# Kernel optimization log

Hardware: AMD Instinct MI355X
Metric: run time of the kernel (lower is better)

Reference implementation:

```python
import jax, jax.numpy as jnp
import numpy as np

N = 6144       # nodes
E = 98304      # edges (~16 per node)
D = 256        # input_dim
K = 20         # max_clusters
NUM_LVS = 32   # distinct LV group ids
MIN_SIZE = 3.0
MAX_SIZE = 20.0


def _lv_constraint_table():
    # Static per-LV preferred-cluster soft constraint (0.3 base, 1.0 preferred).
    max_cpl = max(2, K // max(1, NUM_LVS - 5))
    table = np.ones((NUM_LVS, K), dtype=np.float32)
    for i in range(NUM_LVS):
        start = (i * 2) % K
        end = min(start + max_cpl, K)
        pref = np.zeros(K, dtype=np.float32)
        pref[start:end] = 1.0
        table[i] = 0.3 + 0.7 * pref
    return jnp.asarray(table)

_LV_TABLE = _lv_constraint_table()


def _apply_size_constraints(S):
    cs = S.sum(axis=0)  # soft cluster sizes [K]
    pen = jnp.zeros_like(cs)
    pen = jnp.where(cs > MAX_SIZE, -jnp.log(cs / MAX_SIZE + 1e-8), pen)
    pen = jnp.where((cs > 0) & (cs < MIN_SIZE), -0.5 * jnp.log(cs / MIN_SIZE + 1e-8), pen)
    S_adj = jax.nn.softmax(jnp.log(S + 1e-8) + pen[None, :], axis=1)
    very_over = cs > MAX_SIZE * 1.5
    for k in range(K):  # K is small & static; sequential like the original
        col = S_adj[:, k]
        thr = jnp.quantile(col, 0.7)
        weak = (col < thr) & very_over[k]
        S_adj = S_adj.at[:, k].set(jnp.where(weak, 0.0, col))
        rs = jnp.sum(jnp.abs(S_adj), axis=1, keepdims=True)
        S_adj = jnp.where(weak[:, None], S_adj / jnp.maximum(rs, 1e-12), S_adj)
    return jnp.where(jnp.any(pen != 0.0), S_adj, S)


def _hard_rebalance(S):
    n = S.shape[0]
    for _ in range(5):  # fixed max_iterations (early-break is a no-op via masks)
        cs = S.sum(axis=0)  # stale within the k-loop, as in the original
        very_over = cs > MAX_SIZE
        for k in range(K):
            excess = cs[k] - MAX_SIZE
            active = very_over[k] & (excess > 0)
            col = S[:, k]
            num = jnp.minimum(jnp.ceil(excess).astype(jnp.int32) + 5, n)
            order = jnp.argsort(col)  # ascending: weakest first
            ranks = jnp.zeros((n,), jnp.int32).at[order].set(jnp.arange(n, dtype=jnp.int32))
            weak = (ranks < num) & active
            S = S.at[:, k].set(jnp.where(weak, 1e-8, col))
            avail = jnp.clip(MAX_SIZE - cs, 0.0, None)
            w = avail / (avail.sum() + 1e-8)
            S = jnp.where(weak[:, None], S + w[None, :] * S[:, k:k + 1], S)
            rs = jnp.sum(jnp.abs(S), axis=1, keepdims=True)
            S = jnp.where(weak[:, None], S / jnp.maximum(rs, 1e-12), S)
    return S


def _forward(x, edge_index, lv_group_ids, W1, b1, W2, b2, W3, b3, We1, be1, We2, be2):
    n = x.shape[0]
    # assign_net (dropout is identity in eval)
    h = jax.nn.relu(x @ W1 + b1)
    h = jax.nn.relu(h @ W2 + b2)
    logits = h @ W3 + b3  # [N, K]

    # LV mask: values in {0.3, 1.0}; masked_fill only triggers on exact zeros (kept faithful)
    lv_sizes = jax.ops.segment_sum(jnp.ones((n,), logits.dtype), lv_group_ids, num_segments=NUM_LVS)
    big = (lv_sizes > 30.0)[lv_group_ids]
    lv_mask = jnp.where(big[:, None], _LV_TABLE[lv_group_ids], 1.0)
    logits = jnp.where(lv_mask == 0.0, -1e9, logits)

    # load-balancing regularization (reconstructed; source truncated)
    S_soft = jax.nn.softmax(logits, axis=1)
    target = n / K
    logits = logits - 0.1 * (S_soft.sum(axis=0) - target)[None, :] / target

    S = jax.nn.softmax(logits, axis=1)
    S = _apply_size_constraints(S)
    S = _hard_rebalance(S)

    x_embed = jax.nn.relu(x @ We1 + be1) @ We2 + be2
    x_pooled = S.T @ x_embed  # [K, D]

    adj = jnp.zeros((n, n), x.dtype).at[edge_index[0], edge_index[1]].set(1.0)
    adj_pooled = S.T @ adj @ S  # [K, K]

    # link prediction loss: BCE(S S^T, adj) with torch's log clamp at -100
    p = jnp.clip(S @ S.T, 0.0, 1.0)
    logp = jnp.maximum(jnp.log(p), -100.0)
    log1mp = jnp.maximum(jnp.log1p(-p), -100.0)
    link_loss = -jnp.mean(adj * logp + (1.0 - adj) * log1mp)

    entropy_loss = -jnp.mean(jnp.sum(S * jnp.log(S + 1e-8), axis=1))
    balance_loss = jnp.mean(jnp.abs(S.sum(axis=0) - target)) / target
    aux = link_loss + 0.1 * entropy_loss + 0.5 * balance_loss
    return x_pooled, adj_pooled, S, aux


def setup_inputs() -> dict:
    key = jax.random.key(0)
    ks = jax.random.split(key, 8)
    x = jax.random.normal(ks[0], (N, D), jnp.float32)
    edge_index = jax.random.randint(ks[1], (2, E), 0, N)
    lv_group_ids = jax.random.randint(ks[2], (N,), 0, NUM_LVS)

    def lin(k, fi, fo):
        k1, k2 = jax.random.split(k)
        lim = 1.0 / np.sqrt(fi)
        return (jax.random.uniform(k1, (fi, fo), jnp.float32, -lim, lim),
                jax.random.uniform(k2, (fo,), jnp.float32, -lim, lim))

    W1, b1 = lin(ks[3], D, D // 2)
    W2, b2 = lin(ks[4], D // 2, D // 4)
    W3 = jax.random.normal(ks[5], (D // 4, K), jnp.float32) * 0.1  # _init_balanced_assignment
    b3 = jnp.zeros((K,), jnp.float32)
    We1, be1 = lin(ks[6], D, D)
    We2, be2 = lin(ks[7], D, D)
    return dict(x=x, edge_index=edge_index, lv_group_ids=lv_group_ids,
                W1=W1, b1=b1, W2=W2, b2=b2, W3=W3, b3=b3,
                We1=We1, be1=be1, We2=We2, be2=be2)


def reference(x, edge_index, lv_group_ids, W1, b1, W2, b2, W3, b3, We1, be1, We2, be2):
    return _forward(x, edge_index, lv_group_ids, W1, b1, W2, b2, W3, b3, We1, be1, We2, be2)
```

## Files before the change

kernel.cpp:

```cpp
#include <hip/hip_runtime.h>
#include <math.h>

#define N_NODES 6144
#define KCL 20
#define NE 98304
#define RPT 6

#define OFF_BITMAP   491520ull
#define OFF_COLSUM0  5210112ull
#define OFF_CSG      5210192ull
#define OFF_CSFIN    5210272ull
#define OFF_DACC     5210368ull
#define OFF_TICK     5210400ull
#define HDR_BYTES    296ull
#define OFF_LOGITS   5210624ull
#define OFF_WEAK     5235200ull
#define OFF_CSS      5358080ull
#define OFF_TOTZ     5358160ull
#define OFF_UCM      5702144ull
#define OFF_XE       6685184ull
#define OFF_GOUT     13001216ull
#define OFF_RWS      13025792ull

__global__ __launch_bounds__(128) void k_mlp(const float* __restrict__ x,
    const float* __restrict__ W1, const float* __restrict__ b1,
    const float* __restrict__ W2, const float* __restrict__ b2,
    const float* __restrict__ W3, const float* __restrict__ b3,
    float* __restrict__ logits, float* __restrict__ colsum0,
    unsigned* __restrict__ bitmap, float* __restrict__ outHead){
  __shared__ float xs[16][256];
  __shared__ float h1[16][128];
  __shared__ float h2[16][64];
  __shared__ float logitsL[16][20];
  __shared__ float csL[20];
  const int tid = threadIdx.x;
  const int r0 = blockIdx.x * 16;
  { uint4* bm4 = (uint4*)bitmap;
    const int base = blockIdx.x*128 + tid;
    const uint4 z = make_uint4(0u,0u,0u,0u);
    #pragma unroll
    for (int i=0;i<6;i++) bm4[base + i*49152] = z; }
  if (blockIdx.x==0){ for (int i=tid;i<5520;i+=128) outHead[i]=0.f; }
  if (tid < 20) csL[tid]=0.f;
  for (int idx = tid; idx < 16*256; idx += 128){ int u = idx >> 8, i = idx & 255; xs[u][i] = x[(r0+u)*256 + i]; }
  __syncthreads();
  {
    float acc[16]; float bb = b1[tid];
    #pragma unroll
    for (int u=0;u<16;u++) acc[u]=bb;
    for (int i=0;i<256;i++){ float wv = W1[i*128+tid];
      #pragma unroll
      for (int u=0;u<16;u++) acc[u]=fmaf(xs[u][i], wv, acc[u]); }
    #pragma unroll
    for (int u=0;u<16;u++) h1[u][tid]=fmaxf(acc[u],0.f);
  }
  __syncthreads();
  if (tid < 64){
    float acc[16]; float bb = b2[tid];
    #pragma unroll
    for (int u=0;u<16;u++) acc[u]=bb;
    for (int i=0;i<128;i++){ float wv = W2[i*64+tid];
      #pragma unroll
      for (int u=0;u<16;u++) acc[u]=fmaf(h1[u][i], wv, acc[u]); }
    #pragma unroll
    for (int u=0;u<16;u++) h2[u][tid]=fmaxf(acc[u],0.f);
  }
  __syncthreads();
  if (tid < 20){
    float acc[16]; float bb = b3[tid];
    #pragma unroll
    for (int u=0;u<16;u++) acc[u]=bb;
    for (int i=0;i<64;i++){ float wv = W3[i*20+tid];
      #pragma unroll
      for (int u=0;u<16;u++) acc[u]=fmaf(h2[u][i], wv, acc[u]); }
    #pragma unroll
    for (int u=0;u<16;u++){ logits[(r0+u)*20+tid]=acc[u]; logitsL[u][tid]=acc[u]; }
  }
  __syncthreads();
  if (tid < 16){
    float y[20]; float m=-INFINITY;
    #pragma unroll
    for (int c=0;c<20;c++){ y[c]=logitsL[tid][c]; m=fmaxf(m,y[c]); }
    float s=0.f;
    #pragma unroll
    for (int c=0;c<20;c++){ y[c]=expf(y[c]-m); s+=y[c]; }
    #pragma unroll
    for (int c=0;c<20;c++) atomicAdd(&csL[c], y[c]/s);
  }
  __syncthreads();
  if (tid < 20) atomicAdd(&colsum0[tid], csL[tid]);
}

__global__ __launch_bounds__(256) void k_sm2cm(const float* __restrict__ logits, const float* __restrict__ colsum0,
    float* __restrict__ Ucm, float* __restrict__ csG){
  __shared__ float adjv[20]; __shared__ float csL[20];
  const int tid = threadIdx.x;
  if (tid < 20){ adjv[tid] = (0.1f*(colsum0[tid]-307.2f))/307.2f; csL[tid]=0.f; }
  __syncthreads();
  const int r = blockIdx.x*256 + tid;
  float y[20]; float m=-INFINITY;
  const float4* lp = (const float4*)(logits + r*20);
  #pragma unroll
  for (int q=0;q<5;q++){ float4 f=lp[q]; y[q*4]=f.x; y[q*4+1]=f.y; y[q*4+2]=f.z; y[q*4+3]=f.w; }
  #pragma unroll
  for (int c=0;c<20;c++){ y[c]=y[c]-adjv[c]; m=fmaxf(m,y[c]); }
  float s=0.f;
  #pragma unroll
  for (int c=0;c<20;c++){ y[c]=expf(y[c]-m); s+=y[c]; }
  #pragma unroll
  for (int c=0;c<20;c++){ float v=y[c]/s; Ucm[c*6144+r]=v; atomicAdd(&csL[c], v); }
  __syncthreads();
  if (tid < 20) atomicAdd(&csG[tid], csL[tid]);
}

__global__ __launch_bounds__(256) void k_prep(const float* __restrict__ csG,
    float* __restrict__ Ucm, float* __restrict__ Rws){
  const int r = blockIdx.x*256 + threadIdx.x;
  float pen[20]; int flag=0;
  #pragma unroll
  for (int c=0;c<20;c++){ float cc=csG[c]; float p=0.f;
    if (cc > 20.0f) p = -logf(cc/20.0f + 1e-8f);
    if (cc > 0.0f && cc < 3.0f) p = -0.5f*logf(cc/3.0f + 1e-8f);
    pen[c]=p; if (p != 0.f) flag=1; }
  float y[20];
  #pragma unroll
  for (int c=0;c<20;c++) y[c]=Ucm[c*6144+r];
  float ts=0.f;
  if (flag){
    float m2=-INFINITY;
    #pragma unroll
    for (int c=0;c<20;c++){ y[c]=logf(y[c]+1e-8f)+pen[c]; m2=fmaxf(m2,y[c]); }
    float s2=0.f;
    #pragma unroll
    for (int c=0;c<20;c++){ y[c]=expf(y[c]-m2); s2+=y[c]; }
    #pragma unroll
    for (int c=0;c<20;c++){ float vv=y[c]/s2; Ucm[c*6144+r]=vv; ts+=vv; }
  } else {
    #pragma unroll
    for (int c=0;c<20;c++) ts+=y[c];
  }
  Rws[r]=ts;
}


__device__ __forceinline__ void load6(const float* p, float* v){
  const float2* q = (const float2*)p;
  float2 a=q[0], b=q[1], c=q[2];
  v[0]=a.x; v[1]=a.y; v[2]=b.x; v[3]=b.y; v[4]=c.x; v[5]=c.y;
}

struct MidShared {
  unsigned hist[2048*8];
  unsigned pad[3000];
  double wred[16*20];
  int wT20[16][20]; int wB20[16][20]; int totZ20[20];
  float csGs[20]; float csS[20];
  unsigned st[8];
  alignas(16) unsigned wMin[16];
  alignas(16) int wS[16];
};

__device__ __forceinline__ int blockExclScan16(int val, int tid, int lane, int wv,
                                               int* wS, int* totOut){
  __syncthreads();
  int inc = val;
  for (int off=1;off<64;off<<=1){ int nv=__shfl_up(inc,off); if (lane>=off) inc+=nv; }
  if (lane==63) wS[wv]=inc;
  __syncthreads();
  int4 a=*(int4*)&wS[0], b=*(int4*)&wS[4], c=*(int4*)&wS[8], d=*(int4*)&wS[12];
  int tot = a.x+a.y+a.z+a.w + b.x+b.y+b.z+b.w + c.x+c.y+c.z+c.w + d.x+d.y+d.z+d.w;
  int base = 0;
  base += (wv> 0)?a.x:0; base += (wv> 1)?a.y:0; base += (wv> 2)?a.z:0; base += (wv> 3)?a.w:0;
  base += (wv> 4)?b.x:0; base += (wv> 5)?b.y:0; base += (wv> 6)?b.z:0; base += (wv> 7)?b.w:0;
  base += (wv> 8)?c.x:0; base += (wv> 9)?c.y:0; base += (wv>10)?c.z:0; base += (wv>11)?c.w:0;
  base += (wv>12)?d.x:0; base += (wv>13)?d.y:0; base += (wv>14)?d.z:0;
  *totOut = tot;
  return base + inc - val;
}

struct SelRes { unsigned kv, below, rankin, ties; };

__device__ SelRes selectKth6(const float* v, int rank0, unsigned* hist,
                             unsigned* st, int* wS, int tid, int lane, int wv){
  unsigned st0=0u, st1=0u, st2=(unsigned)rank0, st3=0u;
  const unsigned rep=(unsigned)(lane&7);
  bool done=false;
  for (int p=0;p<3 && !done;p++){
    const int shift=(p==0)?21:((p==1)?10:0);
    const int bins =(p==2)?1024:2048;
    unsigned bb[RPT];
    #pragma unroll
    for (int u=0;u<RPT;u++){
      unsigned key=__float_as_uint(v[u]);
      bool ok=(p==0);
      if (p==1) ok=((key>>21)==(st0>>21));
      if (p==2) ok=((key>>10)==(st0>>10));
      bb[u]= ok ? ((key>>shift)&(unsigned)(bins-1)) : 0xFFFFFFFFu;
    }
    #pragma unroll
    for (int u=0;u<RPT;u++){
      bool first=(bb[u]!=0xFFFFFFFFu);
      #pragma unroll
      for (int j=0;j<u;j++) first = first && (bb[j]!=bb[u]);
      if (first){
        unsigned cnt=1u;
        #pragma unroll
        for (int j=u+1;j<RPT;j++) cnt += (bb[j]==bb[u]) ? 1u:0u;
        atomicAdd(&hist[(bb[u]<<3)+rep], cnt);
      }
// ... 137 lines not shown
  { float2* gp = (float2*)(G2 + r0);
    gp[0]=make_float2(G[0],G[1]); gp[1]=make_float2(G[2],G[3]); gp[2]=make_float2(G[4],G[5]); }
  { float2* rp = (float2*)(Rws + r0);
    rp[0]=make_float2(R[0],R[1]); rp[1]=make_float2(R[2],R[3]); rp[2]=make_float2(R[4],R[5]); }
}

__device__ void embed_block(MidShared& sm, const float* __restrict__ x,
    const float* __restrict__ We1, const float* __restrict__ be1,
    const float* __restrict__ We2, const float* __restrict__ be2,
    float* __restrict__ xe, int blk){
  float (*xs)[256] = (float (*)[256])(sm.hist);
  float (*h)[256]  = (float (*)[256])(sm.hist + 4096);
  const int tid = threadIdx.x;
  const int col = tid & 255;
  const int ug  = tid >> 8;
  const int r0 = blk * 16;
  { float4* xsf4 = (float4*)xs;
    xsf4[tid] = ((const float4*)(x + r0*256))[tid]; }
  __syncthreads();
  float acc[4];
  { float bb = be1[col];
    #pragma unroll
    for (int u=0;u<4;u++) acc[u]=bb; }
  for (int i=0;i<256;i+=4){
    float w0 = We1[(i+0)*256+col];
    float w1 = We1[(i+1)*256+col];
    float w2 = We1[(i+2)*256+col];
    float w3 = We1[(i+3)*256+col];
    #pragma unroll
    for (int u=0;u<4;u++){
      const float4 xv = *(const float4*)&xs[ug*4+u][i];
      acc[u]=fmaf(xv.x, w0, acc[u]);
      acc[u]=fmaf(xv.y, w1, acc[u]);
      acc[u]=fmaf(xv.z, w2, acc[u]);
      acc[u]=fmaf(xv.w, w3, acc[u]);
    }
  }
  #pragma unroll
  for (int u=0;u<4;u++) h[ug*4+u][col]=fmaxf(acc[u],0.f);
  __syncthreads();
  { float bb = be2[col];
    #pragma unroll
    for (int u=0;u<4;u++) acc[u]=bb; }
  for (int i=0;i<256;i+=4){
    float w0 = We2[(i+0)*256+col];
    float w1 = We2[(i+1)*256+col];
    float w2 = We2[(i+2)*256+col];
    float w3 = We2[(i+3)*256+col];
    #pragma unroll
    for (int u=0;u<4;u++){
      const float4 xv = *(const float4*)&h[ug*4+u][i];
      acc[u]=fmaf(xv.x, w0, acc[u]);
      acc[u]=fmaf(xv.y, w1, acc[u]);
      acc[u]=fmaf(xv.z, w2, acc[u]);
      acc[u]=fmaf(xv.w, w3, acc[u]);
    }
  }
  #pragma unroll
  for (int u=0;u<4;u++) xe[(r0+ug*4+u)*256+col]=acc[u];
}

__global__ __launch_bounds__(1024) void k_midwide(const float* __restrict__ csG,
    float* __restrict__ Rws, float* __restrict__ G2,
    float* __restrict__ Ucm,
    const float* __restrict__ x,
    const float* __restrict__ We1, const float* __restrict__ be1,
    const float* __restrict__ We2, const float* __restrict__ be2,
    float* __restrict__ xe,
    const int* __restrict__ ei, unsigned int* __restrict__ bitmap){
  __shared__ MidShared sm;
  const int blk = blockIdx.x;
  if (blk == 0){
    constr_block(sm, csG, Rws, G2, Ucm);
  } else if (blk <= 384){
    embed_block(sm, x, We1, be1, We2, be2, xe, blk-1);
  } else {
    const int e = (blk-385)*1024 + threadIdx.x;
    const int i = ei[e], j = ei[NE+e];
    unsigned bit = (unsigned)i*6144u + (unsigned)j;
    atomicOr(&bitmap[bit >> 5], 1u << (bit & 31u));
  }
}

__global__ __launch_bounds__(1024) void k_rbA(const float* __restrict__ G2,
    const float* __restrict__ Ucm, float* __restrict__ csS, int* __restrict__ totZ,
    unsigned char* __restrict__ weak){
  __shared__ double wredL[16];
  __shared__ int wTL[16];
  const int c = blockIdx.x;
  const int tid = threadIdx.x;
  const int lane = tid & 63, wv = tid >> 6;
  const int r0 = tid*RPT;
  float vv[RPT], g[RPT];
  load6(Ucm + c*6144 + r0, vv);
  load6(G2 + r0, g);
  double d=0.0; int z=0;
  #pragma unroll
  for (int u=0;u<RPT;u++){
    if (vv[u]==0.0f) z++;
    d += (double)__fmul_rn(vv[u], g[u]);
  }
  for (int off=32;off>0;off>>=1) d += __shfl_down(d, off);
  int inc=z;
  for (int off=1;off<64;off<<=1){ int nv=__shfl_up(inc,off); if (lane>=off) inc+=nv; }
  if (lane==0)  wredL[wv]=d;
  if (lane==63) wTL[wv]=inc;
  __syncthreads();
  double s=0.0;
  #pragma unroll
  for (int w2=0;w2<16;w2++) s += wredL[w2];
  const float cs=(float)s;
  int base=0, tz=0;
  #pragma unroll
  for (int w2=0;w2<16;w2++){ int t=wTL[w2]; if (w2<wv) base+=t; tz+=t; }
  int num=(int)ceilf(cs-20.0f)+5; if (num>6144) num=6144;
  const bool act = (cs > 20.0f);
  int rank = base + inc - z;
  #pragma unroll
  for (int u=0;u<RPT;u++){
    bool zb = (vv[u]==0.0f);
    weak[c*6144 + r0 + u] = (act && zb && rank<num) ? (unsigned char)1 : (unsigned char)0;
    if (zb) rank++;
  }
  if (tid==0){ csS[c]=cs; totZ[c]=tz; }
}

__global__ __launch_bounds__(1024) void k_rbC(float* __restrict__ G2,
    float* __restrict__ Rws, float* __restrict__ Ucm,
    const float* __restrict__ csS, const int* __restrict__ totZ,
    const unsigned char* __restrict__ weak){
  __shared__ MidShared sm;
  const int tid = threadIdx.x;
  float csL[20]; float s0=0.f; unsigned actm=0u;
  #pragma unroll
  for (int c=0;c<20;c++){ float cs=csS[c]; csL[c]=cs;
    s0 += fmaxf(20.0f-cs,0.f);
    if (cs > 20.0f) actm |= (1u<<c); }
  const int wzero=(s0==0.0f)?1:0;
  const float wsum=s0+1e-8f;
  const int anyA=(actm!=0u)?1:0;
  int ng=0;
  #pragma unroll
  for (int c=0;c<20;c++){
    if ((actm>>c)&1u){
      int num=(int)ceilf(csL[c]-20.0f)+5; if (num>6144) num=6144;
      if (num > totZ[c]) ng=1;
    }
  }
  if (anyA && !wzero) ng=1;
  if (!anyA) return;
  if (!ng){
    const int r = blockIdx.x*1024 + tid;
    float G=G2[r], R=Rws[r];
    #pragma unroll
    for (int c=0;c<20;c++){
      if (weak[c*6144+r]){
        float Gold = G;
        float t   = __fadd_rn(__fmul_rn(R, Gold), 1e-8f);
        float rsm = fmaxf(t, 1e-12f);
        float un  = __fdiv_rn(1e-8f, Gold);
        Ucm[c*6144+r] = un;
        G = __fdiv_rn(Gold, rsm);
        R = __fadd_rn(R, un);
      }
    }
    G2[r]=G; Rws[r]=R;
  } else {
    if (blockIdx.x!=0) return;
    unsigned* hist = sm.hist; unsigned* st = sm.st; int* wS = sm.wS;
    const int lane = tid & 63, wv = tid >> 6;
    const int r0 = tid*RPT;
    { uint4* h4=(uint4*)hist; const uint4 z=make_uint4(0u,0u,0u,0u);
      #pragma unroll
      for (int i=0;i<4;i++) h4[tid+i*1024]=z; }
    __syncthreads();
    float G[RPT], R[RPT];
    load6(G2 + r0, G);
    load6(Rws + r0, R);
    for (int k=0;k<20;k++){
      if ((actm>>k)&1u){
        float cs=csL[k];
        int num=(int)ceilf(cs-20.0f)+5; if (num>6144) num=6144;
        float u24[RPT];
        load6(Ucm + k*6144 + r0, u24);
        int zc=0;
        #pragma unroll
        for (int u=0;u<RPT;u++) zc += (u24[u]==0.0f) ? 1 : 0;
        int tz2;
        int zBase = blockExclScan16(zc, tid, lane, wv, wS, &tz2);
        bool wk[RPT];
        if (num <= tz2){
          int cnt = zBase;
          #pragma unroll
          for (int u=0;u<RPT;u++){ wk[u]=false; if (u24[u]==0.0f){ if (cnt<num) wk[u]=true; cnt++; } }
        } else {
          float sv24[RPT];
          #pragma unroll
          for (int u=0;u<RPT;u++) sv24[u]=__fmul_rn(u24[u], G[u]);
          SelRes sr = selectKth6(sv24, num-1, hist, st, wS, tid, lane, wv);
          unsigned kV = sr.kv;
          int L = (int)sr.below;
          int Rq = num - L;
          int ec=0;
          #pragma unroll
          for (int u=0;u<RPT;u++) ec += (__float_as_uint(sv24[u])==kV) ? 1 : 0;
          int eTot;
          int eBase = blockExclScan16(ec, tid, lane, wv, wS, &eTot);
          int cnt = eBase;
          #pragma unroll
          for (int u=0;u<RPT;u++){
            unsigned key = __float_as_uint(sv24[u]); wk[u]=false;
            if (key < kV) wk[u]=true;
            else if (key == kV){ if (cnt < Rq) wk[u]=true; cnt++; }
          }
        }
        #pragma unroll
        for (int u=0;u<RPT;u++){
          if (wk[u]){
            const int r = r0+u;
            float rs=0.f; float xv2[20];
            #pragma unroll
            for (int j=0;j<20;j++){
              float xv = (j==k) ? 1e-8f : __fmul_rn(Ucm[j*6144+r], G[u]);
              float wLj = fmaxf(20.0f - csL[j], 0.f) / wsum;
              xv = __fadd_rn(xv, __fmul_rn(wLj, 1e-8f));
              xv2[j]=xv; rs += fabsf(xv);
            }
            float rsm = fmaxf(rs, 1e-12f);
            float nR = 0.f;
            #pragma unroll
            for (int j=0;j<20;j++){
              float nv = __fdiv_rn(xv2[j], rsm);
              Ucm[j*6144+r] = nv; nR += nv;
            }
            G[u]=1.0f; R[u]=nR;
          }
        }
        __syncthreads();
      }
    }
    { float2* gp = (float2*)(G2 + r0);
      gp[0]=make_float2(G[0],G[1]); gp[1]=make_float2(G[2],G[3]); gp[2]=make_float2(G[4],G[5]); }
    { float2* rp = (float2*)(Rws + r0);
      rp[0]=make_float2(R[0],R[1]); rp[1]=make_float2(R[2],R[3]); rp[2]=make_float2(R[4],R[5]); }
  }
}

__global__ __launch_bounds__(256) void k_tail1(const float* __restrict__ Ucm,
    const float* __restrict__ Gout, const float* __restrict__ xe,
    const unsigned* __restrict__ bitmap,
    float* __restrict__ outXP, float* __restrict__ outS,
    float* __restrict__ csfin, double* __restrict__ dAcc,
    float* __restrict__ outAdj, float* __restrict__ outAux,
    unsigned* __restrict__ ticket){
  __shared__ float SiT[256][21];
  __shared__ float SjT[256][21];
  __shared__ float csL[20];
  __shared__ float adjacc[400];
  __shared__ double wsum[4];
  const int tid = threadIdx.x;
  const int blk = blockIdx.x;
  const int lane = tid & 63, wvq = tid >> 6;

  if (blk < 24){
    const int r0 = blk * 256;
    if (tid < 20) csL[tid]=0.f;
    __syncthreads();
    {
      const int r = r0 + tid;
      const float Gr = Gout[r];
      float sv[20]; float ent=0.f;
      #pragma unroll
      for (int c=0;c<20;c++) sv[c]=__fmul_rn(Ucm[c*6144+r], Gr);
      float4* so = (float4*)(outS + r*20);
      #pragma unroll
      for (int q=0;q<5;q++){ float4 f; f.x=sv[q*4]; f.y=sv[q*4+1]; f.z=sv[q*4+2]; f.w=sv[q*4+3]; so[q]=f; }
      #pragma unroll
      for (int c=0;c<20;c++){ SiT[tid][c]=sv[c]; ent += sv[c]*logf(sv[c]+1e-08f); }
      #pragma unroll
      for (int c=0;c<20;c++) atomicAdd(&csL[c], sv[c]);
      double ed = (double)ent;
      for (int off=32;off>0;off>>=1) ed += __shfl_down(ed, off);
      if (lane==0) wsum[wvq]=ed;
    }
    __syncthreads();
    if (tid==0) atomicAdd(&dAcc[2], wsum[0]+wsum[1]+wsum[2]+wsum[3]);
    if (tid<20) atomicAdd(&csfin[tid], csL[tid]);
    float acc[20];
    #pragma unroll
    for (int c=0;c<20;c++) acc[c]=0.f;
    for (int i=0;i<256;i++){
      float xv = xe[(r0+i)*256 + tid];
      #pragma unroll
      for (int c=0;c<20;c++) acc[c]=fmaf(SiT[i][c], xv, acc[c]);
    }
    #pragma unroll
    for (int c=0;c<20;c++) atomicAdd(&outXP[c*256+tid], acc[c]);
  } else if (blk < 120){
    const int rbase = (blk-24)*64 + wvq*16;
    for (int t=tid;t<400;t+=256) adjacc[t]=0.f;
    __syncthreads();
    int c7[7], d7[7], n7=0;
    #pragma unroll
    for (int q=0;q<7;q++){ int e=lane+64*q; if (e<400){ c7[q]=e/20; d7[q]=e%20; n7=q+1; } }
    float acc7[7];
    #pragma unroll
    for (int q=0;q<7;q++) acc7[q]=0.f;
    float eacc = 0.f;
    for (int rr=0; rr<16; rr++){
      const int i = rbase + rr;
      const float Gi = Gout[i];
      float Si[20];
      #pragma unroll
      for (int c=0;c<20;c++) Si[c]=__fmul_rn(Ucm[c*6144+i], Gi);
      float Tp[20];
      #pragma unroll
      for (int c=0;c<20;c++) Tp[c]=0.f;
      #pragma unroll
      for (int w=0; w<3; w++){
        const int wq = lane + w*64;
        unsigned word = bitmap[i*192 + wq];
        while (word){
          int b = __ffs((int)word) - 1; word &= (word-1u);
          int j = wq*32 + b;
          const float Gj = Gout[j];
          float p = 0.f;
          #pragma unroll
          for (int c=0;c<20;c++){
// ... 22 lines not shown
    #pragma unroll
    for (int q=0;q<7;q++){
      if (q < n7) atomicAdd(&adjacc[lane+64*q], acc7[q]);
    }
    double cd = (double)eacc;
    for (int off=32;off>0;off>>=1) cd += __shfl_down(cd, off);
    if (lane==0) wsum[wvq]=cd;
    __syncthreads();
    if (tid==0) atomicAdd(&dAcc[1], wsum[0]+wsum[1]+wsum[2]+wsum[3]);
    for (int t=tid;t<400;t+=256) atomicAdd(&outAdj[t], adjacc[t]);
  } else {
    const int q2 = blk - 120;
    const int ib = (q2/24)*256, jb = (q2%24)*256;
    const float gi = Gout[ib+tid];
    #pragma unroll
    for (int c=0;c<20;c++) SiT[tid][c] = __fmul_rn(Ucm[c*6144+ib+tid], gi);
    const float gj = Gout[jb+tid];
    #pragma unroll
    for (int c=0;c<20;c++) SjT[tid][c] = __fmul_rn(Ucm[c*6144+jb+tid], gj);
    __syncthreads();
    float rA[20];
    #pragma unroll
    for (int c=0;c<20;c++) rA[c]=SiT[tid][c];
    float af = 0.f;
    for (int jj=0;jj<256;jj++){
      float p=0.f;
      #pragma unroll
      for (int c=0;c<20;c++) p = fmaf(rA[c], SjT[jj][c], p);
      float pcl = fminf(fmaxf(p,0.f),1.f);
      af += fmaxf(__logf(1.0f-pcl), -100.f);
    }
    double cd = (double)af;
    for (int off=32;off>0;off>>=1) cd += __shfl_down(cd, off);
    if (lane==0) wsum[wvq]=cd;
    __syncthreads();
    if (tid==0) atomicAdd(&dAcc[0], wsum[0]+wsum[1]+wsum[2]+wsum[3]);
  }

  __syncthreads();
  if (tid==0){
    unsigned t = atomicAdd(ticket, 1u);
    if (t == 695u){
      __threadfence();
      double l0 = __hip_atomic_load(&dAcc[0], __ATOMIC_RELAXED, __HIP_MEMORY_SCOPE_AGENT);
      double l1 = __hip_atomic_load(&dAcc[1], __ATOMIC_RELAXED, __HIP_MEMORY_SCOPE_AGENT);
      double l2 = __hip_atomic_load(&dAcc[2], __ATOMIC_RELAXED, __HIP_MEMORY_SCOPE_AGENT);
      float s=0.f;
      for (int c=0;c<20;c++){
        float cf = __hip_atomic_load(&csfin[c], __ATOMIC_RELAXED, __HIP_MEMORY_SCOPE_AGENT);
        s += fabsf(cf-307.2f);
      }
      const double nsq = 6144.0*6144.0;
      float link = (float)(-(l0+l1)/nsq);
      float ent  = (float)(-(l2/6144.0));
      float bal = (s/20.0f)/307.2f;
      outAux[0] = link + 0.1f*ent + 0.5f*bal;
    }
  }
}

extern "C" void kernel_launch(void* const* d_in, const int* in_sizes, int n_in,
                              void* d_out, int out_size, void* d_ws, size_t ws_size,
                              hipStream_t stream) {
  const float* x   = (const float*)d_in[0];
  const int*   ei  = (const int*)d_in[1];
  const float* W1  = (const float*)d_in[3];
  const float* b1  = (const float*)d_in[4];
  const float* W2  = (const float*)d_in[5];
  const float* b2  = (const float*)d_in[6];
  const float* W3  = (const float*)d_in[7];
  const float* b3  = (const float*)d_in[8];
  const float* We1 = (const float*)d_in[9];
  const float* be1 = (const float*)d_in[10];
  const float* We2 = (const float*)d_in[11];
  const float* be2 = (const float*)d_in[12];

  char* ws = (char*)d_ws;
  unsigned int* bitmap = (unsigned int*)(ws + OFF_BITMAP);
  float* colsum0  = (float*)(ws + OFF_COLSUM0);
  float* csG      = (float*)(ws + OFF_CSG);
  float* csfin    = (float*)(ws + OFF_CSFIN);
  double* dAcc    = (double*)(ws + OFF_DACC);
  unsigned* ticket= (unsigned*)(ws + OFF_TICK);
  float* logits   = (float*)(ws + OFF_LOGITS);
  float* Ucm      = (float*)(ws + OFF_UCM);
  float* xe       = (float*)(ws + OFF_XE);
  float* Rws      = (float*)(ws + OFF_RWS);
  float* G2       = logits;
  unsigned char* weak = (unsigned char*)(ws + OFF_WEAK);
  float* csS      = (float*)(ws + OFF_CSS);
  int*   totZ     = (int*)(ws + OFF_TOTZ);

  float* out   = (float*)d_out;
  float* outXP = out;
  float* outAdj= out + 5120;
  float* outS  = out + 5520;
  float* outAux= out + 128400;

  hipMemsetAsync(ws + OFF_COLSUM0, 0, (size_t)HDR_BYTES, stream);

  k_mlp<<<384, 128, 0, stream>>>(x, W1,b1, W2,b2, W3,b3, logits, colsum0, bitmap, out);
  k_sm2cm<<<24, 256, 0, stream>>>(logits, colsum0, Ucm, csG);
  k_prep<<<24, 256, 0, stream>>>(csG, Ucm, Rws);
  k_midwide<<<481, 1024, 0, stream>>>(csG, Rws, G2, Ucm,
                                      x, We1, be1, We2, be2, xe, ei, bitmap);
  for (int it=0; it<5; ++it){
    k_rbA<<<20, 1024, 0, stream>>>(G2, Ucm, csS, totZ, weak);
    k_rbC<<<6, 1024, 0, stream>>>(G2, Rws, Ucm, csS, totZ, weak);
  }
  k_tail1<<<696, 256, 0, stream>>>(Ucm, G2, xe, bitmap,
                                   outXP, outS, csfin, dAcc, outAdj, outAux, ticket);
}
```

Before: 528.1 us.

## Fuse rebalance loop and softmax/prep kernels using software grid barriers

Replaces the ten small per-iteration rebalance launches with one persistent 20-block kernel that runs all five iterations, using an atomic-counter grid barrier between phases. The softmax and size-penalty prep kernels are likewise merged with a grid barrier, and the softmax values are kept in registers instead of being reloaded from Ucm. The goal is to remove launch overhead and inter-kernel gaps on a latency-bound chain. In exchange it relies on all blocks being co-resident, and spin-waiting adds some cost; the barrier counters are zeroed by the extended header memset.

```diff
diff --git a/kernel.cpp b/kernel.cpp
--- a/kernel.cpp
+++ b/kernel.cpp
@@ -12,14 +12,15 @@
 #define OFF_CSFIN    5210272ull
 #define OFF_DACC     5210368ull
 #define OFF_TICK     5210400ull
-#define HDR_BYTES    296ull
+#define OFF_GBAR     5210404ull
+#define OFF_GBAR2    5210408ull
+#define HDR_BYTES    304ull
 #define OFF_LOGITS   5210624ull
 #define OFF_WEAK     5235200ull
 #define OFF_CSS      5358080ull
 #define OFF_TOTZ     5358160ull
 #define OFF_UCM      5702144ull
 #define OFF_XE       6685184ull
-#define OFF_GOUT     13001216ull
 #define OFF_RWS      13025792ull
 
 __global__ __launch_bounds__(128) void k_mlp(const float* __restrict__ x,
@@ -91,8 +92,9 @@
   if (tid < 20) atomicAdd(&colsum0[tid], csL[tid]);
 }
 
-__global__ __launch_bounds__(256) void k_sm2cm(const float* __restrict__ logits, const float* __restrict__ colsum0,
-    float* __restrict__ Ucm, float* __restrict__ csG){
+__global__ __launch_bounds__(256) void k_sm2p(const float* __restrict__ logits,
+    const float* __restrict__ colsum0, float* __restrict__ Ucm,
+    float* __restrict__ csG, float* __restrict__ Rws, unsigned* __restrict__ gbar2){
   __shared__ float adjv[20]; __shared__ float csL[20];
   const int tid = threadIdx.x;
   if (tid < 20){ adjv[tid] = (0.1f*(colsum0[tid]-307.2f))/307.2f; csL[tid]=0.f; }
@@ -108,23 +110,24 @@
   #pragma unroll
   for (int c=0;c<20;c++){ y[c]=expf(y[c]-m); s+=y[c]; }
   #pragma unroll
-  for (int c=0;c<20;c++){ float v=y[c]/s; Ucm[c*6144+r]=v; atomicAdd(&csL[c], v); }
+  for (int c=0;c<20;c++){ float v=y[c]/s; y[c]=v; Ucm[c*6144+r]=v; atomicAdd(&csL[c], v); }
   __syncthreads();
   if (tid < 20) atomicAdd(&csG[tid], csL[tid]);
-}
-
-__global__ __launch_bounds__(256) void k_prep(const float* __restrict__ csG,
-    float* __restrict__ Ucm, float* __restrict__ Rws){
-  const int r = blockIdx.x*256 + threadIdx.x;
+  __syncthreads();
+  if (tid==0){
+    __threadfence();
+    __hip_atomic_fetch_add(gbar2, 1u, __ATOMIC_RELEASE, __HIP_MEMORY_SCOPE_AGENT);
+    while (__hip_atomic_load(gbar2, __ATOMIC_ACQUIRE, __HIP_MEMORY_SCOPE_AGENT) < 24u)
+      __builtin_amdgcn_s_sleep(2);
+    __threadfence();
+  }
+  __syncthreads();
   float pen[20]; int flag=0;
   #pragma unroll
   for (int c=0;c<20;c++){ float cc=csG[c]; float p=0.f;
     if (cc > 20.0f) p = -logf(cc/20.0f + 1e-8f);
     if (cc > 0.0f && cc < 3.0f) p = -0.5f*logf(cc/3.0f + 1e-8f);
     pen[c]=p; if (p != 0.f) flag=1; }
-  float y[20];
-  #pragma unroll
-  for (int c=0;c<20;c++) y[c]=Ucm[c*6144+r];
   float ts=0.f;
   if (flag){
     float m2=-INFINITY;
@@ -428,167 +431,185 @@
   }
 }
 
-__global__ __launch_bounds__(1024) void k_rbA(const float* __restrict__ G2,
-    const float* __restrict__ Ucm, float* __restrict__ csS, int* __restrict__ totZ,
-    unsigned char* __restrict__ weak){
+__device__ __forceinline__ void gridbar20(unsigned* gbar, unsigned target){
+  __syncthreads();
+  if (threadIdx.x==0){
+    __threadfence();
+    __hip_atomic_fetch_add(gbar, 1u, __ATOMIC_RELEASE, __HIP_MEMORY_SCOPE_AGENT);
+    while (__hip_atomic_load(gbar, __ATOMIC_ACQUIRE, __HIP_MEMORY_SCOPE_AGENT) < target)
+      __builtin_amdgcn_s_sleep(4);
+    __threadfence();
+  }
+  __syncthreads();
+}
+
+__global__ __launch_bounds__(1024) void k_rebal5(float* __restrict__ G2,
+    float* __restrict__ Rws, float* __restrict__ Ucm,
+    float* __restrict__ csS, int* __restrict__ totZ,
+    unsigned char* __restrict__ weak, unsigned* __restrict__ gbar){
+  __shared__ MidShared sm;
   __shared__ double wredL[16];
   __shared__ int wTL[16];
-  const int c = blockIdx.x;
   const int tid = threadIdx.x;
   const int lane = tid & 63, wv = tid >> 6;
-  const int r0 = tid*RPT;
-  float vv[RPT], g[RPT];
-  load6(Ucm + c*6144 + r0, vv);
-  load6(G2 + r0, g);
-  double d=0.0; int z=0;
-  #pragma unroll
-  for (int u=0;u<RPT;u++){
-    if (vv[u]==0.0f) z++;
-    d += (double)__fmul_rn(vv[u], g[u]);
-  }
-  for (int off=32;off>0;off>>=1) d += __shfl_down(d, off);
-  int inc=z;
-  for (int off=1;off<64;off<<=1){ int nv=__shfl_up(inc,off); if (lane>=off) inc+=nv; }
-  if (lane==0)  wredL[wv]=d;
-  if (lane==63) wTL[wv]=inc;
-  __syncthreads();
-  double s=0.0;
-  #pragma unroll
-  for (int w2=0;w2<16;w2++) s += wredL[w2];
-  const float cs=(float)s;
-  int base=0, tz=0;
-  #pragma unroll
-  for (int w2=0;w2<16;w2++){ int t=wTL[w2]; if (w2<wv) base+=t; tz+=t; }
-  int num=(int)ceilf(cs-20.0f)+5; if (num>6144) num=6144;
-  const bool act = (cs > 20.0f);
-  int rank = base + inc - z;
-  #pragma unroll
-  for (int u=0;u<RPT;u++){
-    bool zb = (vv[u]==0.0f);
-    weak[c*6144 + r0 + u] = (act && zb && rank<num) ? (unsigned char)1 : (unsigned char)0;
-    if (zb) rank++;
-  }
-  if (tid==0){ csS[c]=cs; totZ[c]=tz; }
-}
-
-__global__ __launch_bounds__(1024) void k_rbC(float* __restrict__ G2,
-    float* __restrict__ Rws, float* __restrict__ Ucm,
-    const float* __restrict__ csS, const int* __restrict__ totZ,
-    const unsigned char* __restrict__ weak){
-  __shared__ MidShared sm;
-  const int tid = threadIdx.x;
-  float csL[20]; float s0=0.f; unsigned actm=0u;
-  #pragma unroll
-  for (int c=0;c<20;c++){ float cs=csS[c]; csL[c]=cs;
-    s0 += fmaxf(20.0f-cs,0.f);
-    if (cs > 20.0f) actm |= (1u<<c); }
-  const int wzero=(s0==0.0f)?1:0;
-  const float wsum=s0+1e-8f;
-  const int anyA=(actm!=0u)?1:0;
-  int ng=0;
-  #pragma unroll
-  for (int c=0;c<20;c++){
-    if ((actm>>c)&1u){
-      int num=(int)ceilf(csL[c]-20.0f)+5; if (num>6144) num=6144;
-      if (num > totZ[c]) ng=1;
-    }
-  }
-  if (anyA && !wzero) ng=1;
-  if (!anyA) return;
-  if (!ng){
-    const int r = blockIdx.x*1024 + tid;
-    float G=G2[r], R=Rws[r];
+  const int blk = blockIdx.x;
+  unsigned bar = 0;
+
+  for (int it=0; it<5; ++it){
+    {
+      const int c = blk;
+      const int r0 = tid*RPT;
+      float vv[RPT], g[RPT];
+      load6(Ucm + c*6144 + r0, vv);
+      load6(G2 + r0, g);
+      double d=0.0; int z=0;
+      #pragma unroll
+      for (int u=0;u<RPT;u++){
+        if (vv[u]==0.0f) z++;
+        d += (double)__fmul_rn(vv[u], g[u]);
+      }
+      for (int off=32;off>0;off>>=1) d += __shfl_down(d, off);
+      int inc=z;
+      for (int off=1;off<64;off<<=1){ int nv=__shfl_up(inc,off); if (lane>=off) inc+=nv; }
+      if (lane==0)  wredL[wv]=d;
+      if (lane==63) wTL[wv]=inc;
+      __syncthreads();
+      double s=0.0;
+      #pragma unroll
+      for (int w2=0;w2<16;w2++) s += wredL[w2];
+      const float cs=(float)s;
+      int base=0, tz=0;
+      #pragma unroll
+      for (int w2=0;w2<16;w2++){ int t=wTL[w2]; if (w2<wv) base+=t; tz+=t; }
+      int num=(int)ceilf(cs-20.0f)+5; if (num>6144) num=6144;
+      const bool act = (cs > 20.0f);
+      int rank = base + inc - z;
+      #pragma unroll
+      for (int u=0;u<RPT;u++){
+        bool zb = (vv[u]==0.0f);
+        weak[c*6144 + r0 + u] = (act && zb && rank<num) ? (unsigned char)1 : (unsigned char)0;
+        if (zb) rank++;
+      }
+      if (tid==0){ csS[c]=cs; totZ[c]=tz; }
+      __syncthreads();
+    }
+    bar++; gridbar20(gbar, bar*20u);
+
+    float csL2[20]; float s0=0.f; unsigned actm=0u;
+    #pragma unroll
+    for (int c=0;c<20;c++){ float cs=csS[c]; csL2[c]=cs;
+      s0 += fmaxf(20.0f-cs,0.f);
+      if (cs > 20.0f) actm |= (1u<<c); }
+    const int wzero=(s0==0.0f)?1:0;
+    const float wsum=s0+1e-8f;
+    const int anyA=(actm!=0u)?1:0;
+    int ng=0;
     #pragma unroll
     for (int c=0;c<20;c++){
-      if (weak[c*6144+r]){
-        float Gold = G;
-        float t   = __fadd_rn(__fmul_rn(R, Gold), 1e-8f);
-        float rsm = fmaxf(t, 1e-12f);
-        float un  = __fdiv_rn(1e-8f, Gold);
-        Ucm[c*6144+r] = un;
-        G = __fdiv_rn(Gold, rsm);
-        R = __fadd_rn(R, un);
-      }
-    }
-    G2[r]=G; Rws[r]=R;
-  } else {
-    if (blockIdx.x!=0) return;
-    unsigned* hist = sm.hist; unsigned* st = sm.st; int* wS = sm.wS;
-    const int lane = tid & 63, wv = tid >> 6;
-    const int r0 = tid*RPT;
-    { uint4* h4=(uint4*)hist; const uint4 z=make_uint4(0u,0u,0u,0u);
-      #pragma unroll
-      for (int i=0;i<4;i++) h4[tid+i*1024]=z; }
-    __syncthreads();
-    float G[RPT], R[RPT];
-    load6(G2 + r0, G);
-    load6(Rws + r0, R);
-    for (int k=0;k<20;k++){
-      if ((actm>>k)&1u){
-        float cs=csL[k];
-        int num=(int)ceilf(cs-20.0f)+5; if (num>6144) num=6144;
-        float u24[RPT];
-        load6(Ucm + k*6144 + r0, u24);
-        int zc=0;
+      if ((actm>>c)&1u){
+        int num=(int)ceilf(csL2[c]-20.0f)+5; if (num>6144) num=6144;
+        if (num > totZ[c]) ng=1;
+      }
+    }
+    if (anyA && !wzero) ng=1;
+    if (!anyA) break;
+
+    if (!ng){
+      if (blk < 6){
+        const int r = blk*1024 + tid;
+        float G=G2[r], R=Rws[r];
         #pragma unroll
-        for (int u=0;u<RPT;u++) zc += (u24[u]==0.0f) ? 1 : 0;
-        int tz2;
-        int zBase = blockExclScan16(zc, tid, lane, wv, wS, &tz2);
-        bool wk[RPT];
-        if (num <= tz2){
-          int cnt = zBase;
+        for (int c=0;c<20;c++){
+          if (weak[c*6144+r]){
+            float Gold = G;
+            float t   = __fadd_rn(__fmul_rn(R, Gold), 1e-8f);
+            float rsm = fmaxf(t, 1e-12f);
+            float un  = __fdiv_rn(1e-8f, Gold);
+            Ucm[c*6144+r] = un;
+            G = __fdiv_rn(Gold, rsm);
+            R = __fadd_rn(R, un);
+          }
+        }
+        G2[r]=G; Rws[r]=R;
+      }
+    } else if (blk==0){
+      unsigned* hist = sm.hist; unsigned* st = sm.st; int* wS = sm.wS;
+      const int r0 = tid*RPT;
+      { uint4* h4=(uint4*)hist; const uint4 z=make_uint4(0u,0u,0u,0u);
+        #pragma unroll
+        for (int i=0;i<4;i++) h4[tid+i*1024]=z; }
+      __syncthreads();
+      float G[RPT], R[RPT];
+      load6(G2 + r0, G);
+      load6(Rws + r0, R);
+      for (int k=0;k<20;k++){
+        if ((actm>>k)&1u){
+          float cs=csL2[k];
+          int num=(int)ceilf(cs-20.0f)+5; if (num>6144) num=6144;
+          float u24[RPT];
+          load6(Ucm + k*6144 + r0, u24);
+          int zc=0;
           #pragma unroll
-          for (int u=0;u<RPT;u++){ wk[u]=false; if (u24[u]==0.0f){ if (cnt<num) wk[u]=true; cnt++; } }
-        } else {
-          float sv24[RPT];
-          #pragma unroll
-          for (int u=0;u<RPT;u++) sv24[u]=__fmul_rn(u24[u], G[u]);
-          SelRes sr = selectKth6(sv24, num-1, hist, st, wS, tid, lane, wv);
-          unsigned kV = sr.kv;
-          int L = (int)sr.below;
-          int Rq = num - L;
-          int ec=0;
-          #pragma unroll
-          for (int u=0;u<RPT;u++) ec += (__float_as_uint(sv24[u])==kV) ? 1 : 0;
-          int eTot;
-          int eBase = blockExclScan16(ec, tid, lane, wv, wS, &eTot);
-          int cnt = eBase;
+          for (int u=0;u<RPT;u++) zc += (u24[u]==0.0f) ? 1 : 0;
+          int tz2;
+          int zBase = blockExclScan16(zc, tid, lane, wv, wS, &tz2);
+          bool wk[RPT];
+          if (num <= tz2){
+            int cnt = zBase;
+            #pragma unroll
+            for (int u=0;u<RPT;u++){ wk[u]=false; if (u24[u]==0.0f){ if (cnt<num) wk[u]=true; cnt++; } }
+          } else {
+            float sv24[RPT];
+            #pragma unroll
+            for (int u=0;u<RPT;u++) sv24[u]=__fmul_rn(u24[u], G[u]);
+            SelRes sr = selectKth6(sv24, num-1, hist, st, wS, tid, lane, wv);
+            unsigned kV = sr.kv;
+            int L = (int)sr.below;
+            int Rq = num - L;
+            int ec=0;
+            #pragma unroll
+            for (int u=0;u<RPT;u++) ec += (__float_as_uint(sv24[u])==kV) ? 1 : 0;
+            int eTot;
+            int eBase = blockExclScan16(ec, tid, lane, wv, wS, &eTot);
+            int cnt = eBase;
+            #pragma unroll
+            for (int u=0;u<RPT;u++){
+              unsigned key = __float_as_uint(sv24[u]); wk[u]=false;
+              if (key < kV) wk[u]=true;
+              else if (key == kV){ if (cnt < Rq) wk[u]=true; cnt++; }
+            }
+          }
           #pragma unroll
           for (int u=0;u<RPT;u++){
-            unsigned key = __float_as_uint(sv24[u]); wk[u]=false;
-            if (key < kV) wk[u]=true;
-            else if (key == kV){ if (cnt < Rq) wk[u]=true; cnt++; }
+            if (wk[u]){
+              const int r = r0+u;
+              float rs=0.f; float xv2[20];
+              #pragma unroll
+              for (int j=0;j<20;j++){
+                float xv = (j==k) ? 1e-8f : __fmul_rn(Ucm[j*6144+r], G[u]);
+                float wLj = fmaxf(20.0f - csL2[j], 0.f) / wsum;
+                xv = __fadd_rn(xv, __fmul_rn(wLj, 1e-8f));
+                xv2[j]=xv; rs += fabsf(xv);
+              }
+              float rsm = fmaxf(rs, 1e-12f);
+              float nR = 0.f;
+              #pragma unroll
+              for (int j=0;j<20;j++){
+                float nv = __fdiv_rn(xv2[j], rsm);
+                Ucm[j*6144+r] = nv; nR += nv;
+              }
+              G[u]=1.0f; R[u]=nR;
+            }
           }
+          __syncthreads();
         }
-        #pragma unroll
-        for (int u=0;u<RPT;u++){
-          if (wk[u]){
-            const int r = r0+u;
-            float rs=0.f; float xv2[20];
-            #pragma unroll
-            for (int j=0;j<20;j++){
-              float xv = (j==k) ? 1e-8f : __fmul_rn(Ucm[j*6144+r], G[u]);
-              float wLj = fmaxf(20.0f - csL[j], 0.f) / wsum;
-              xv = __fadd_rn(xv, __fmul_rn(wLj, 1e-8f));
-              xv2[j]=xv; rs += fabsf(xv);
-            }
-            float rsm = fmaxf(rs, 1e-12f);
-            float nR = 0.f;
-            #pragma unroll
-            for (int j=0;j<20;j++){
-              float nv = __fdiv_rn(xv2[j], rsm);
-              Ucm[j*6144+r] = nv; nR += nv;
-            }
-            G[u]=1.0f; R[u]=nR;
-          }
-        }
-        __syncthreads();
-      }
-    }
-    { float2* gp = (float2*)(G2 + r0);
-      gp[0]=make_float2(G[0],G[1]); gp[1]=make_float2(G[2],G[3]); gp[2]=make_float2(G[4],G[5]); }
-    { float2* rp = (float2*)(Rws + r0);
-      rp[0]=make_float2(R[0],R[1]); rp[1]=make_float2(R[2],R[3]); rp[2]=make_float2(R[4],R[5]); }
+      }
+      { float2* gp = (float2*)(G2 + r0);
+        gp[0]=make_float2(G[0],G[1]); gp[1]=make_float2(G[2],G[3]); gp[2]=make_float2(G[4],G[5]); }
+      { float2* rp = (float2*)(Rws + r0);
+        rp[0]=make_float2(R[0],R[1]); rp[1]=make_float2(R[2],R[3]); rp[2]=make_float2(R[4],R[5]); }
+    }
+    if (it < 4){ bar++; gridbar20(gbar, bar*20u); }
   }
 }
 
@@ -778,6 +799,8 @@
   float* csfin    = (float*)(ws + OFF_CSFIN);
   double* dAcc    = (double*)(ws + OFF_DACC);
   unsigned* ticket= (unsigned*)(ws + OFF_TICK);
+  unsigned* gbar  = (unsigned*)(ws + OFF_GBAR);
+  unsigned* gbar2 = (unsigned*)(ws + OFF_GBAR2);
   float* logits   = (float*)(ws + OFF_LOGITS);
   float* Ucm      = (float*)(ws + OFF_UCM);
   float* xe       = (float*)(ws + OFF_XE);
@@ -796,14 +819,10 @@
   hipMemsetAsync(ws + OFF_COLSUM0, 0, (size_t)HDR_BYTES, stream);
 
   k_mlp<<<384, 128, 0, stream>>>(x, W1,b1, W2,b2, W3,b3, logits, colsum0, bitmap, out);
-  k_sm2cm<<<24, 256, 0, stream>>>(logits, colsum0, Ucm, csG);
-  k_prep<<<24, 256, 0, stream>>>(csG, Ucm, Rws);
+  k_sm2p<<<24, 256, 0, stream>>>(logits, colsum0, Ucm, csG, Rws, gbar2);
   k_midwide<<<481, 1024, 0, stream>>>(csG, Rws, G2, Ucm,
                                       x, We1, be1, We2, be2, xe, ei, bitmap);
-  for (int it=0; it<5; ++it){
-    k_rbA<<<20, 1024, 0, stream>>>(G2, Ucm, csS, totZ, weak);
-    k_rbC<<<6, 1024, 0, stream>>>(G2, Rws, Ucm, csS, totZ, weak);
-  }
+  k_rebal5<<<20, 1024, 0, stream>>>(G2, Rws, Ucm, csS, totZ, weak, gbar);
   k_tail1<<<696, 256, 0, stream>>>(Ucm, G2, xe, bitmap,
                                    outXP, outS, csfin, dAcc, outAdj, outAux, ticket);
 }
```

Result: slower. 620.5 us (+17.5%).

## Collapse five rebalance iterations into one rank-bucketed pass

Applied to the files above, without the earlier changes.

The five-iteration rebalance loop (10 kernel launches) is replaced by one ranking kernel and one apply kernel. The ranking kernel labels each zero entry with the iteration it would be evicted in (rank/num). The fast path then replays those evictions in iteration order per row, on the assumption that column sums stay unchanged across iterations. A single-block fallback recomputes all five iterations in-kernel when that assumption might not hold. This removes launch and synchronisation overhead between iterations, but relies on a subtle equivalence that could break if cluster sizes shift between iterations.

```diff
diff --git a/kernel.cpp b/kernel.cpp
--- a/kernel.cpp
+++ b/kernel.cpp
@@ -430,7 +430,7 @@
 
 __global__ __launch_bounds__(1024) void k_rbA(const float* __restrict__ G2,
     const float* __restrict__ Ucm, float* __restrict__ csS, int* __restrict__ totZ,
-    unsigned char* __restrict__ weak){
+    unsigned char* __restrict__ weakIt){
   __shared__ double wredL[16];
   __shared__ int wTL[16];
   const int c = blockIdx.x;
@@ -465,16 +465,18 @@
   #pragma unroll
   for (int u=0;u<RPT;u++){
     bool zb = (vv[u]==0.0f);
-    weak[c*6144 + r0 + u] = (act && zb && rank<num) ? (unsigned char)1 : (unsigned char)0;
+    unsigned char wi = 255;
+    if (act && zb && rank < 5*num) wi = (unsigned char)(rank / num);
+    weakIt[c*6144 + r0 + u] = wi;
     if (zb) rank++;
   }
   if (tid==0){ csS[c]=cs; totZ[c]=tz; }
 }
 
-__global__ __launch_bounds__(1024) void k_rbC(float* __restrict__ G2,
-    float* __restrict__ Rws, float* __restrict__ Ucm,
+__global__ __launch_bounds__(1024) void k_rbB(const float* __restrict__ G2,
+    const float* __restrict__ Rws, float* __restrict__ Ucm, float* __restrict__ Gout,
     const float* __restrict__ csS, const int* __restrict__ totZ,
-    const unsigned char* __restrict__ weak){
+    const unsigned char* __restrict__ weakIt){
   __shared__ MidShared sm;
   const int tid = threadIdx.x;
   float csL[20]; float s0=0.f; unsigned actm=0u;
@@ -485,32 +487,41 @@
   const int wzero=(s0==0.0f)?1:0;
   const float wsum=s0+1e-8f;
   const int anyA=(actm!=0u)?1:0;
-  int ng=0;
+  int fastok = wzero;
   #pragma unroll
   for (int c=0;c<20;c++){
     if ((actm>>c)&1u){
       int num=(int)ceilf(csL[c]-20.0f)+5; if (num>6144) num=6144;
-      if (num > totZ[c]) ng=1;
-    }
-  }
-  if (anyA && !wzero) ng=1;
-  if (!anyA) return;
-  if (!ng){
+      if (5*num > totZ[c]) fastok=0;
+    }
+  }
+  if (!anyA){
+    const int r = blockIdx.x*1024 + tid;
+    Gout[r] = G2[r];
+    return;
+  }
+  if (fastok){
     const int r = blockIdx.x*1024 + tid;
     float G=G2[r], R=Rws[r];
-    #pragma unroll
-    for (int c=0;c<20;c++){
-      if (weak[c*6144+r]){
-        float Gold = G;
-        float t   = __fadd_rn(__fmul_rn(R, Gold), 1e-8f);
-        float rsm = fmaxf(t, 1e-12f);
-        float un  = __fdiv_rn(1e-8f, Gold);
-        Ucm[c*6144+r] = un;
-        G = __fdiv_rn(Gold, rsm);
-        R = __fadd_rn(R, un);
-      }
-    }
-    G2[r]=G; Rws[r]=R;
+    unsigned char wi[20];
+    #pragma unroll
+    for (int c=0;c<20;c++) wi[c]=weakIt[c*6144+r];
+    #pragma unroll
+    for (int i=0;i<5;i++){
+      #pragma unroll
+      for (int c=0;c<20;c++){
+        if (wi[c]==(unsigned char)i){
+          float Gold = G;
+          float t   = __fadd_rn(__fmul_rn(R, Gold), 1e-8f);
+          float rsm = fmaxf(t, 1e-12f);
+          float un  = __fdiv_rn(1e-8f, Gold);
+          Ucm[c*6144+r] = un;
+          G = __fdiv_rn(Gold, rsm);
+          R = __fadd_rn(R, un);
+        }
+      }
+    }
+    Gout[r]=G;
   } else {
     if (blockIdx.x!=0) return;
     unsigned* hist = sm.hist; unsigned* st = sm.st; int* wS = sm.wS;
@@ -523,73 +534,158 @@
     float G[RPT], R[RPT];
     load6(G2 + r0, G);
     load6(Rws + r0, R);
-    for (int k=0;k<20;k++){
-      if ((actm>>k)&1u){
-        float cs=csL[k];
-        int num=(int)ceilf(cs-20.0f)+5; if (num>6144) num=6144;
-        float u24[RPT];
-        load6(Ucm + k*6144 + r0, u24);
-        int zc=0;
+    for (int it=0; it<5; it++){
+      int zb2[RPT];
+      #pragma unroll
+      for (int u=0;u<RPT;u++) zb2[u]=0;
+      for (int c=0;c<20;c++){
+        float vv[RPT];
+        load6(Ucm + c*6144 + r0, vv);
+        double d=0.0;
         #pragma unroll
-        for (int u=0;u<RPT;u++) zc += (u24[u]==0.0f) ? 1 : 0;
-        int tz2;
-        int zBase = blockExclScan16(zc, tid, lane, wv, wS, &tz2);
-        bool wk[RPT];
-        if (num <= tz2){
-          int cnt = zBase;
-          #pragma unroll
-          for (int u=0;u<RPT;u++){ wk[u]=false; if (u24[u]==0.0f){ if (cnt<num) wk[u]=true; cnt++; } }
-        } else {
-          float sv24[RPT];
-          #pragma unroll
-          for (int u=0;u<RPT;u++) sv24[u]=__fmul_rn(u24[u], G[u]);
-          SelRes sr = selectKth6(sv24, num-1, hist, st, wS, tid, lane, wv);
-          unsigned kV = sr.kv;
-          int L = (int)sr.below;
-          int Rq = num - L;
-          int ec=0;
-          #pragma unroll
-          for (int u=0;u<RPT;u++) ec += (__float_as_uint(sv24[u])==kV) ? 1 : 0;
-          int eTot;
-          int eBase = blockExclScan16(ec, tid, lane, wv, wS, &eTot);
-          int cnt = eBase;
-          #pragma unroll
-          for (int u=0;u<RPT;u++){
-            unsigned key = __float_as_uint(sv24[u]); wk[u]=false;
-            if (key < kV) wk[u]=true;
-            else if (key == kV){ if (cnt < Rq) wk[u]=true; cnt++; }
+        for (int u=0;u<RPT;u++){
+          if (vv[u]==0.0f) zb2[u] |= (1<<c);
+          d += (double)__fmul_rn(vv[u], G[u]);
+        }
+        for (int off=32;off>0;off>>=1) d += __shfl_down(d, off);
+        if (lane==0) sm.wred[wv*20+c]=d;
+      }
+      __syncthreads();
+      if (tid<20){ double s=0.0; for (int w2=0;w2<16;w2++) s += sm.wred[w2*20+tid]; sm.csS[tid]=(float)s; }
+      __syncthreads();
+      float t0=0.f; unsigned am=0u;
+      #pragma unroll
+      for (int c=0;c<20;c++){
+        float cs=sm.csS[c];
+        t0 += fmaxf(20.0f-cs,0.f);
+        if (cs > 20.0f) am |= (1u<<c);
+      }
+      const int wz = (t0==0.0f) ? 1 : 0;
+      const float ws2 = t0 + 1e-8f;
+      int exc2[20];
+      #pragma unroll
+      for (int c=0;c<20;c++){
+        int z=0;
+        #pragma unroll
+        for (int u=0;u<RPT;u++) z += (zb2[u]>>c)&1;
+        int inc = z;
+        for (int off=1;off<64;off<<=1){ int nv=__shfl_up(inc,off); if (lane>=off) inc+=nv; }
+        if (lane==63) sm.wT20[wv][c]=inc;
+        exc2[c]=inc-z;
+      }
+      __syncthreads();
+      if (tid<20){
+        int run=0;
+        for (int w2=0;w2<16;w2++){ sm.wB20[w2][tid]=run; run+=sm.wT20[w2][tid]; }
+        sm.totZ20[tid]=run;
+      }
+      __syncthreads();
+      const int aa = (am!=0u) ? 1 : 0;
+      int ng=0;
+      #pragma unroll
+      for (int c=0;c<20;c++){
+        if ((am>>c)&1u){
+          float cs=sm.csS[c];
+          int num=(int)ceilf(cs-20.0f)+5; if (num>6144) num=6144;
+          if (num > sm.totZ20[c]) ng=1;
+        }
+      }
+      if (aa && !wz) ng=1;
+      if (!aa) continue;
+      if (!ng){
+        #pragma unroll
+        for (int c=0;c<20;c++){
+          if ((am>>c)&1u){
+            float cs=sm.csS[c];
+            int num=(int)ceilf(cs-20.0f)+5; if (num>6144) num=6144;
+            int rank = sm.wB20[wv][c] + exc2[c];
+            #pragma unroll
+            for (int u=0;u<RPT;u++){
+              if ((zb2[u]>>c)&1){
+                if (rank < num){
+                  float Gold = G[u];
+                  float t   = __fadd_rn(__fmul_rn(R[u], Gold), 1e-8f);
+                  float rsm = fmaxf(t, 1e-12f);
+                  float un  = __fdiv_rn(1e-8f, Gold);
+                  Ucm[c*6144+r0+u] = un;
+                  G[u] = __fdiv_rn(Gold, rsm);
+                  R[u] = __fadd_rn(R[u], un);
+                }
+                rank++;
+              }
+            }
           }
         }
-        #pragma unroll
-        for (int u=0;u<RPT;u++){
-          if (wk[u]){
-            const int r = r0+u;
-            float rs=0.f; float xv2[20];
+      } else {
+        for (int k=0;k<20;k++){
+          if ((am>>k)&1u){
+            float cs=sm.csS[k];
+            int num=(int)ceilf(cs-20.0f)+5; if (num>6144) num=6144;
+            float u24[RPT];
+            load6(Ucm + k*6144 + r0, u24);
+            int zc=0;
             #pragma unroll
-            for (int j=0;j<20;j++){
-              float xv = (j==k) ? 1e-8f : __fmul_rn(Ucm[j*6144+r], G[u]);
-              float wLj = fmaxf(20.0f - csL[j], 0.f) / wsum;
-              xv = __fadd_rn(xv, __fmul_rn(wLj, 1e-8f));
-              xv2[j]=xv; rs += fabsf(xv);
+            for (int u=0;u<RPT;u++) zc += (u24[u]==0.0f) ? 1 : 0;
+            int tz2;
+            int zBase = blockExclScan16(zc, tid, lane, wv, wS, &tz2);
+            bool wk[RPT];
+            if (num <= tz2){
+              int cnt = zBase;
+              #pragma unroll
+              for (int u=0;u<RPT;u++){ wk[u]=false; if (u24[u]==0.0f){ if (cnt<num) wk[u]=true; cnt++; } }
+            } else {
+              float sv24[RPT];
+              #pragma unroll
+              for (int u=0;u<RPT;u++) sv24[u]=__fmul_rn(u24[u], G[u]);
+              SelRes sr = selectKth6(sv24, num-1, hist, st, wS, tid, lane, wv);
+              unsigned kV = sr.kv;
+              int L = (int)sr.below;
+              int Rq = num - L;
+              int ec=0;
+              #pragma unroll
+              for (int u=0;u<RPT;u++) ec += (__float_as_uint(sv24[u])==kV) ? 1 : 0;
+              int eTot;
+              int eBase = blockExclScan16(ec, tid, lane, wv, wS, &eTot);
+              int cnt = eBase;
+              #pragma unroll
+              for (int u=0;u<RPT;u++){
+                unsigned key = __float_as_uint(sv24[u]); wk[u]=false;
+                if (key < kV) wk[u]=true;
+                else if (key == kV){ if (cnt < Rq) wk[u]=true; cnt++; }
+              }
             }
-            float rsm = fmaxf(rs, 1e-12f);
-            float nR = 0.f;
             #pragma unroll
-            for (int j=0;j<20;j++){
-              float nv = __fdiv_rn(xv2[j], rsm);
-              Ucm[j*6144+r] = nv; nR += nv;
+            for (int u=0;u<RPT;u++){
+              if (wk[u]){
+                const int r = r0+u;
+                float rs=0.f; float xv2[20];
+                #pragma unroll
+                for (int j=0;j<20;j++){
+                  float xv = (j==k) ? 1e-8f : __fmul_rn(Ucm[j*6144+r], G[u]);
+                  float wLj = fmaxf(20.0f - sm.csS[j], 0.f) / ws2;
+                  xv = __fadd_rn(xv, __fmul_rn(wLj, 1e-8f));
+                  xv2[j]=xv; rs += fabsf(xv);
+                }
+                float rsm = fmaxf(rs, 1e-12f);
+                float nR = 0.f;
+                #pragma unroll
+                for (int j=0;j<20;j++){
+                  float nv = __fdiv_rn(xv2[j], rsm);
+                  Ucm[j*6144+r] = nv; nR += nv;
+                }
+                G[u]=1.0f; R[u]=nR;
+              }
             }
-            G[u]=1.0f; R[u]=nR;
+            __syncthreads();
           }
         }
         __syncthreads();
       }
     }
-    { float2* gp = (float2*)(G2 + r0);
+    { float2* gp = (float2*)(Gout + r0);
       gp[0]=make_float2(G[0],G[1]); gp[1]=make_float2(G[2],G[3]); gp[2]=make_float2(G[4],G[5]); }
-    { float2* rp = (float2*)(Rws + r0);
-      rp[0]=make_float2(R[0],R[1]); rp[1]=make_float2(R[2],R[3]); rp[2]=make_float2(R[4],R[5]); }
-  }
+  }
+  (void)wsum;
 }
 
 __global__ __launch_bounds__(256) void k_tail1(const float* __restrict__ Ucm,
@@ -781,9 +877,10 @@
   float* logits   = (float*)(ws + OFF_LOGITS);
   float* Ucm      = (float*)(ws + OFF_UCM);
   float* xe       = (float*)(ws + OFF_XE);
+  float* Gout     = (float*)(ws + OFF_GOUT);
   float* Rws      = (float*)(ws + OFF_RWS);
   float* G2       = logits;
-  unsigned char* weak = (unsigned char*)(ws + OFF_WEAK);
+  unsigned char* weakIt = (unsigned char*)(ws + OFF_WEAK);
   float* csS      = (float*)(ws + OFF_CSS);
   int*   totZ     = (int*)(ws + OFF_TOTZ);
 
@@ -800,10 +897,8 @@
   k_prep<<<24, 256, 0, stream>>>(csG, Ucm, Rws);
   k_midwide<<<481, 1024, 0, stream>>>(csG, Rws, G2, Ucm,
                                       x, We1, be1, We2, be2, xe, ei, bitmap);
-  for (int it=0; it<5; ++it){
-    k_rbA<<<20, 1024, 0, stream>>>(G2, Ucm, csS, totZ, weak);
-    k_rbC<<<6, 1024, 0, stream>>>(G2, Rws, Ucm, csS, totZ, weak);
-  }
-  k_tail1<<<696, 256, 0, stream>>>(Ucm, G2, xe, bitmap,
+  k_rbA<<<20, 1024, 0, stream>>>(G2, Ucm, csS, totZ, weakIt);
+  k_rbB<<<6, 1024, 0, stream>>>(G2, Rws, Ucm, Gout, csS, totZ, weakIt);
+  k_tail1<<<696, 256, 0, stream>>>(Ucm, Gout, xe, bitmap,
                                    outXP, outS, csfin, dAcc, outAdj, outAux, ticket);
 }
```

Result: faster. 469.4 us (-11.1%).
